# Kernel tuning notes

Measured on AMD Instinct MI355X. Metric: run time of the kernel, lower is better.

The kernel has to match this reference:

```python
import jax, jax.numpy as jnp
import numpy as np

B, L, DIN, DOUT = 256, 2048, 128, 128


def setup_inputs() -> dict:
    key = jax.random.key(0)
    ks = jax.random.split(key, 5)
    lim = float(np.sqrt(6.0 / (DIN + DOUT)))
    x = jax.random.normal(ks[0], (B, L, DIN), jnp.float32)
    u_w = jax.random.uniform(ks[1], (DOUT, DIN), jnp.float32, -lim, lim)
    u_b = jnp.zeros((DOUT,), jnp.float32)
    g_w = jax.random.uniform(ks[2], (DOUT, DIN + DOUT), jnp.float32, -lim, lim)
    g_b = jnp.zeros((DOUT,), jnp.float32)
    a_w = jax.random.uniform(ks[3], (DOUT, DIN + DOUT), jnp.float32, -lim, lim)
    s0 = jax.random.normal(ks[4], (DOUT,), jnp.float32)
    return {"x": x, "s0": s0, "u_w": u_w, "u_b": u_b, "g_w": g_w, "g_b": g_b, "a_w": a_w}


def reference(x, s0, u_w, u_b, g_w, g_b, a_w):
    # x: [B, L, DIN] (shape_mode='blc')
    Bsz = x.shape[0]
    # Split concat-weights: Linear([x, h]) == x @ Wx.T + h @ Wh.T (+ b)
    g_wx, g_wh = g_w[:, :DIN], g_w[:, DIN:]
    a_wx, a_wh = a_w[:, :DIN], a_w[:, DIN:]

    # Precompute all x-dependent projections as batched GEMMs: [B, L, DOUT]
    U = jnp.einsum('bld,od->blo', x, u_w) + u_b
    Gx = jnp.einsum('bld,od->blo', x, g_wx) + g_b
    Ax = jnp.einsum('bld,od->blo', x, a_wx)

    last_h0 = jnp.tanh(jnp.broadcast_to(s0, (Bsz, DOUT)))
    num0 = jnp.zeros((Bsz, DOUT), x.dtype)
    den0 = jnp.zeros((Bsz, DOUT), x.dtype)
    a_max0 = jnp.full((Bsz, DOUT), 1e-38, x.dtype)

    def step(carry, inp):
        num, den, last_h, last_a_max = carry
        ui, gx, ax = inp  # each [B, DOUT]
        g = jnp.tanh(gx + last_h @ g_wh.T)
        z = ui * g
        a = ax + last_h @ a_wh.T
        a_max = jnp.maximum(a, last_a_max)  # == max over stack([a, last_a_max])
        e_to_a = jnp.exp(a_max - last_a_max)  # faithful to source (as written)
        num = num + z * e_to_a
        den = den + e_to_a
        h = jnp.tanh(num / den)
        return (num, den, h, a_max), h

    xs = (jnp.swapaxes(U, 0, 1), jnp.swapaxes(Gx, 0, 1), jnp.swapaxes(Ax, 0, 1))
    _, hs = jax.lax.scan(step, (num0, den0, last_h0, a_max0), xs)
    return jnp.swapaxes(hs, 0, 1)  # [B, L, DOUT]
```

## Files before the change

### kernel.cpp

```cpp
#include <hip/hip_runtime.h>

#define BB 256
#define LL 2048
#define DIN 128
#define DOUT 128
#define T 32
#define TT 16

__device__ __forceinline__ float tanh_fast(float v) {
    float e = __expf(2.0f * v);
    return 1.0f - 2.0f / (e + 1.0f);
}

__global__ __launch_bounds__(256, 1)
void rwa_fused(const float* __restrict__ x, const float* __restrict__ s0,
               const float* __restrict__ u_w, const float* __restrict__ u_b,
               const float* __restrict__ g_w, const float* __restrict__ g_b,
               const float* __restrict__ a_w, float* __restrict__ out)
{
    __shared__ float x_sh[T * DIN];
    __shared__ float pU[T * DOUT];
    __shared__ float pG[T * DOUT];
    __shared__ float pA[T * DOUT];
    __shared__ float h_sh[DOUT];
    __shared__ float alin_sh[DOUT];

    const int tid = threadIdx.x;
    const int o   = tid & 127;
    const int grp = tid >> 7;
    const int b   = blockIdx.x;

    float4 wreg[32];
    {
        const float* wbase = (grp == 0 ? g_w : a_w) + (size_t)o * (DIN + DOUT) + DIN;
        const float4* wsrc = (const float4*)wbase;
        #pragma unroll
        for (int i = 0; i < 32; i++) wreg[i] = wsrc[i];
    }
    const float ub = u_b[o];
    const float gb = g_b[o];

    float num = 0.0f, den = 0.0f, amax = 1e-38f;
    if (tid < DOUT) h_sh[tid] = tanh_fast(s0[tid]);
    __syncthreads();

    const float4* u4 = (const float4*)(u_w + (size_t)o * DIN);
    const float4* g4 = (const float4*)(g_w + (size_t)o * (DIN + DOUT));
    const float4* a4 = (const float4*)(a_w + (size_t)o * (DIN + DOUT));

    for (int t0 = 0; t0 < LL; t0 += T) {
        {
            const float4* xg = (const float4*)(x + ((size_t)b * LL + t0) * DIN);
            float4* xs = (float4*)x_sh;
            #pragma unroll
            for (int i = 0; i < (T * DIN / 4) / 256; i++)
                xs[tid + 256 * i] = xg[tid + 256 * i];
        }
        __syncthreads();

        {
            float accU[TT], accG[TT], accA[TT];
            #pragma unroll
            for (int tt = 0; tt < TT; tt++) { accU[tt] = ub; accG[tt] = gb; accA[tt] = 0.0f; }
            const float4* xs4 = (const float4*)x_sh + (size_t)(grp * TT) * 32;
            #pragma unroll 2
            for (int k4 = 0; k4 < 32; k4++) {
                float4 wu = u4[k4], wg = g4[k4], wa = a4[k4];
                #pragma unroll
                for (int tt = 0; tt < TT; tt++) {
                    float4 xv = xs4[tt * 32 + k4];
                    accU[tt] = fmaf(wu.x, xv.x, fmaf(wu.y, xv.y, fmaf(wu.z, xv.z, fmaf(wu.w, xv.w, accU[tt]))));
                    accG[tt] = fmaf(wg.x, xv.x, fmaf(wg.y, xv.y, fmaf(wg.z, xv.z, fmaf(wg.w, xv.w, accG[tt]))));
                    accA[tt] = fmaf(wa.x, xv.x, fmaf(wa.y, xv.y, fmaf(wa.z, xv.z, fmaf(wa.w, xv.w, accA[tt]))));
                }
            }
            #pragma unroll
            for (int tt = 0; tt < TT; tt++) {
                int t = grp * TT + tt;
                pU[t * DOUT + o] = accU[tt];
                pG[t * DOUT + o] = accG[tt];
                pA[t * DOUT + o] = accA[tt];
            }
        }
        __syncthreads();

        for (int ts = 0; ts < T; ts++) {
            float ax0 = 0.f, ax1 = 0.f, ax2 = 0.f, ax3 = 0.f;
            const float4* h4 = (const float4*)h_sh;
            #pragma unroll
            for (int k4 = 0; k4 < 32; k4++) {
                float4 hv = h4[k4];
                ax0 = fmaf(wreg[k4].x, hv.x, ax0);
                ax1 = fmaf(wreg[k4].y, hv.y, ax1);
                ax2 = fmaf(wreg[k4].z, hv.z, ax2);
                ax3 = fmaf(wreg[k4].w, hv.w, ax3);
            }
            float dot = (ax0 + ax1) + (ax2 + ax3);
            if (grp == 1) alin_sh[o] = dot;
            __syncthreads();
            if (grp == 0) {
                float g = tanh_fast(pG[ts * DOUT + o] + dot);
                float z = pU[ts * DOUT + o] * g;
                float a = pA[ts * DOUT + o] + alin_sh[o];
                float amn = fmaxf(a, amax);
                float e = __expf(amn - amax);
                amax = amn;
                num = fmaf(z, e, num);
                den += e;
                float h = tanh_fast(num / den);
                h_sh[o] = h;
                out[((size_t)b * LL + (t0 + ts)) * DOUT + o] = h;
            }
            __syncthreads();
        }
    }
}

extern "C" void kernel_launch(void* const* d_in, const int* in_sizes, int n_in,
                              void* d_out, int out_size, void* d_ws, size_t ws_size,
                              hipStream_t stream) {
    const float* x   = (const float*)d_in[0];
    const float* s0  = (const float*)d_in[1];
    const float* u_w = (const float*)d_in[2];
    const float* u_b = (const float*)d_in[3];
    const float* g_w = (const float*)d_in[4];
    const float* g_b = (const float*)d_in[5];
    const float* a_w = (const float*)d_in[6];
    float* out = (float*)d_out;
    rwa_fused<<<BB, 256, 0, stream>>>(x, s0, u_w, u_b, g_w, g_b, a_w, out);
}
```

Before: 3.611 ms.

## Split recurrent dot products across 512 threads and stage outputs for coalesced stores

Doubles the block to 512 threads so each thread computes half of the hidden-state dot product for the gate or attention weights. Partial sums are combined through shared memory. Each step's output is buffered in shared memory and written per tile with coalesced float4 stores instead of per-step scalar stores. This shortens the serial per-step latency, at the cost of an extra shared-memory reduction and more threads hitting the barriers.

```diff
diff --git a/kernel.cpp b/kernel.cpp
--- a/kernel.cpp
+++ b/kernel.cpp
@@ -5,14 +5,15 @@
 #define DIN 128
 #define DOUT 128
 #define T 32
-#define TT 16
+#define NTHREADS 512
+#define TT 8
 
 __device__ __forceinline__ float tanh_fast(float v) {
     float e = __expf(2.0f * v);
     return 1.0f - 2.0f / (e + 1.0f);
 }
 
-__global__ __launch_bounds__(256, 1)
+__global__ __launch_bounds__(NTHREADS, 2)
 void rwa_fused(const float* __restrict__ x, const float* __restrict__ s0,
                const float* __restrict__ u_w, const float* __restrict__ u_b,
                const float* __restrict__ g_w, const float* __restrict__ g_b,
@@ -23,19 +24,22 @@
     __shared__ float pG[T * DOUT];
     __shared__ float pA[T * DOUT];
     __shared__ float h_sh[DOUT];
-    __shared__ float alin_sh[DOUT];
+    __shared__ float psum[3 * DOUT];
 
-    const int tid = threadIdx.x;
-    const int o   = tid & 127;
-    const int grp = tid >> 7;
-    const int b   = blockIdx.x;
+    const int tid  = threadIdx.x;
+    const int o    = tid & 127;
+    const int sel  = tid >> 7;
+    const int side = sel >> 1;
+    const int half = sel & 1;
+    const int b    = blockIdx.x;
 
-    float4 wreg[32];
+    float4 wreg[16];
     {
-        const float* wbase = (grp == 0 ? g_w : a_w) + (size_t)o * (DIN + DOUT) + DIN;
+        const float* wbase = (side == 0 ? g_w : a_w)
+                           + (size_t)o * (DIN + DOUT) + DIN + half * 64;
         const float4* wsrc = (const float4*)wbase;
         #pragma unroll
-        for (int i = 0; i < 32; i++) wreg[i] = wsrc[i];
+        for (int i = 0; i < 16; i++) wreg[i] = wsrc[i];
     }
     const float ub = u_b[o];
     const float gb = g_b[o];
@@ -53,8 +57,8 @@
             const float4* xg = (const float4*)(x + ((size_t)b * LL + t0) * DIN);
             float4* xs = (float4*)x_sh;
             #pragma unroll
-            for (int i = 0; i < (T * DIN / 4) / 256; i++)
-                xs[tid + 256 * i] = xg[tid + 256 * i];
+            for (int i = 0; i < (T * DIN / 4) / NTHREADS; i++)
+                xs[tid + NTHREADS * i] = xg[tid + NTHREADS * i];
         }
         __syncthreads();
 
@@ -62,7 +66,7 @@
             float accU[TT], accG[TT], accA[TT];
             #pragma unroll
             for (int tt = 0; tt < TT; tt++) { accU[tt] = ub; accG[tt] = gb; accA[tt] = 0.0f; }
-            const float4* xs4 = (const float4*)x_sh + (size_t)(grp * TT) * 32;
+            const float4* xs4 = (const float4*)x_sh + (size_t)(sel * TT) * 32;
             #pragma unroll 2
             for (int k4 = 0; k4 < 32; k4++) {
                 float4 wu = u4[k4], wg = g4[k4], wa = a4[k4];
@@ -76,7 +80,7 @@
             }
             #pragma unroll
             for (int tt = 0; tt < TT; tt++) {
-                int t = grp * TT + tt;
+                int t = sel * TT + tt;
                 pU[t * DOUT + o] = accU[tt];
                 pG[t * DOUT + o] = accG[tt];
                 pA[t * DOUT + o] = accA[tt];
@@ -85,23 +89,27 @@
         __syncthreads();
 
         for (int ts = 0; ts < T; ts++) {
+            float4 hv[16];
+            const float4* h4 = (const float4*)h_sh + half * 16;
+            #pragma unroll
+            for (int i = 0; i < 16; i++) hv[i] = h4[i];
             float ax0 = 0.f, ax1 = 0.f, ax2 = 0.f, ax3 = 0.f;
-            const float4* h4 = (const float4*)h_sh;
             #pragma unroll
-            for (int k4 = 0; k4 < 32; k4++) {
-                float4 hv = h4[k4];
-                ax0 = fmaf(wreg[k4].x, hv.x, ax0);
-                ax1 = fmaf(wreg[k4].y, hv.y, ax1);
-                ax2 = fmaf(wreg[k4].z, hv.z, ax2);
-                ax3 = fmaf(wreg[k4].w, hv.w, ax3);
+            for (int i = 0; i < 16; i++) {
+                ax0 = fmaf(wreg[i].x, hv[i].x, ax0);
+                ax1 = fmaf(wreg[i].y, hv[i].y, ax1);
+                ax2 = fmaf(wreg[i].z, hv[i].z, ax2);
+                ax3 = fmaf(wreg[i].w, hv[i].w, ax3);
             }
-            float dot = (ax0 + ax1) + (ax2 + ax3);
-            if (grp == 1) alin_sh[o] = dot;
+            float part = (ax0 + ax1) + (ax2 + ax3);
+            if (sel != 0) psum[(sel - 1) * DOUT + o] = part;
             __syncthreads();
-            if (grp == 0) {
-                float g = tanh_fast(pG[ts * DOUT + o] + dot);
+            if (sel == 0) {
+                float gdot = part + psum[o];
+                float adot = psum[DOUT + o] + psum[2 * DOUT + o];
+                float g = tanh_fast(pG[ts * DOUT + o] + gdot);
                 float z = pU[ts * DOUT + o] * g;
-                float a = pA[ts * DOUT + o] + alin_sh[o];
+                float a = pA[ts * DOUT + o] + adot;
                 float amn = fmaxf(a, amax);
                 float e = __expf(amn - amax);
                 amax = amn;
@@ -109,9 +117,17 @@
                 den += e;
                 float h = tanh_fast(num / den);
                 h_sh[o] = h;
-                out[((size_t)b * LL + (t0 + ts)) * DOUT + o] = h;
+                pU[ts * DOUT + o] = h;
             }
             __syncthreads();
+        }
+
+        {
+            float4* og = (float4*)(out + ((size_t)b * LL + t0) * DOUT);
+            const float4* hs = (const float4*)pU;
+            #pragma unroll
+            for (int i = 0; i < (T * DOUT / 4) / NTHREADS; i++)
+                og[tid + NTHREADS * i] = hs[tid + NTHREADS * i];
         }
     }
 }
@@ -127,5 +143,5 @@
     const float* g_b = (const float*)d_in[5];
     const float* a_w = (const float*)d_in[6];
     float* out = (float*)d_out;
-    rwa_fused<<<BB, 256, 0, stream>>>(x, s0, u_w, u_b, g_w, g_b, a_w, out);
+    rwa_fused<<<BB, NTHREADS, 0, stream>>>(x, s0, u_w, u_b, g_w, g_b, a_w, out);
 }
```

Result: faster. 3.000 ms (-16.9%).
